# Kernel tuning notes

Measured on AMD Instinct MI355X. Metric: run time of the kernel, lower is better.

The kernel has to match this reference:

```python
import jax, jax.numpy as jnp
import numpy as np

N_NODES = 100000
N_EDGES = 1600000
IN_C = 64
OUT_C = 64
BN_EPS = 1e-5


def setup_inputs() -> dict:
    key = jax.random.key(0)
    k1, k2, k3, k4 = jax.random.split(key, 4)
    x = jax.random.normal(k1, (N_NODES, IN_C), dtype=jnp.float32)
    edge_index = jax.random.randint(k2, (2, N_EDGES), 0, N_NODES, dtype=jnp.int64)
    # GCNConv linear: weight [out, in], bias [out] (PyG default has bias=True)
    W = jax.random.normal(k3, (OUT_C, IN_C), dtype=jnp.float32) / np.sqrt(IN_C)
    b = jax.random.normal(k4, (OUT_C,), dtype=jnp.float32) * 0.01
    # BatchNorm1d affine params
    gamma = jnp.ones((OUT_C,), dtype=jnp.float32)
    beta = jnp.zeros((OUT_C,), dtype=jnp.float32)
    return {"x": x, "edge_index": edge_index, "W": W, "b": b, "gamma": gamma, "beta": beta}


def reference(x, edge_index, W, b, gamma, beta):
    N = x.shape[0]
    # GCNConv: linear transform (no bias yet)
    h = x @ W.T  # [N, out]
    # add self-loops
    loop = jnp.arange(N, dtype=edge_index.dtype)
    src = jnp.concatenate([edge_index[0], loop])  # [E+N]
    dst = jnp.concatenate([edge_index[1], loop])
    # symmetric normalization: deg computed on destination (col)
    ones = jnp.ones(src.shape[0], dtype=h.dtype)
    deg = jax.ops.segment_sum(ones, dst, num_segments=N)  # [N]
    deg_inv_sqrt = jnp.where(deg > 0, jax.lax.rsqrt(deg), 0.0)
    norm = deg_inv_sqrt[src] * deg_inv_sqrt[dst]  # [E+N]
    # gather -> scale -> scatter-add aggregation
    msgs = h[src] * norm[:, None]  # [E+N, out] (dominant memory traffic)
    out = jax.ops.segment_sum(msgs, dst, num_segments=N) + b  # [N, out]
    # BatchNorm1d (training mode: biased batch statistics over nodes)
    mean = out.mean(axis=0)
    var = out.var(axis=0)  # biased, matching torch BN normalization
    y = (out - mean) * jax.lax.rsqrt(var + BN_EPS) * gamma + beta
    return jax.nn.relu(y)
```

## Files before the change

### kernel.cpp

```cpp
#include <hip/hip_runtime.h>
#include <math.h>

#define N_NODES 100000
#define N_EDGES 1600000
#define C 64
#define BN_EPS 1e-5f
#define SLOTS 48

#define WS_HP    0
#define WS_CNT   3200000
#define WS_STAT  3300000
#define WS_SLOT  3300128

#define NPART 8
#define PART_NODES (N_NODES / NPART)
#define NCHUNK 128
#define CHUNK_I4 (N_EDGES / 4 / NCHUNK)

typedef float f4 __attribute__((ext_vector_type(4)));

static __device__ __forceinline__ unsigned short f2bf(float f) {
    unsigned u = __float_as_uint(f);
    unsigned r = 0x7FFFu + ((u >> 16) & 1u);
    return (unsigned short)((u + r) >> 16);
}
static __device__ __forceinline__ float bf2f(unsigned short h) {
    return __uint_as_float(((unsigned)h) << 16);
}

__global__ void r16_scatter(const int* __restrict__ ei, unsigned* __restrict__ cnt,
                            unsigned* __restrict__ slot) {
    const int p  = blockIdx.x & (NPART - 1);
    const int ch = blockIdx.x >> 3;
    const unsigned lo = (unsigned)(p * PART_NODES);
    const unsigned hi = lo + PART_NODES;
    const int4* s4 = reinterpret_cast<const int4*>(ei);
    const int4* d4 = reinterpret_cast<const int4*>(ei + N_EDGES);
    const int beg = ch * CHUNK_I4;
    const int end = beg + CHUNK_I4;
    for (int e = beg + threadIdx.x; e < end; e += 256) {
        int4 d = d4[e];
        int4 s = s4[e];
        unsigned dx = (unsigned)d.x, dy = (unsigned)d.y;
        unsigned dz = (unsigned)d.z, dw = (unsigned)d.w;
        if (dx >= lo && dx < hi) {
            unsigned pos = atomicAdd(&cnt[dx], 1u);
            if (pos < SLOTS) slot[dx * SLOTS + pos] = (unsigned)s.x;
        }
        if (dy >= lo && dy < hi) {
            unsigned pos = atomicAdd(&cnt[dy], 1u);
            if (pos < SLOTS) slot[dy * SLOTS + pos] = (unsigned)s.y;
        }
        if (dz >= lo && dz < hi) {
            unsigned pos = atomicAdd(&cnt[dz], 1u);
            if (pos < SLOTS) slot[dz * SLOTS + pos] = (unsigned)s.z;
        }
        if (dw >= lo && dw < hi) {
            unsigned pos = atomicAdd(&cnt[dw], 1u);
            if (pos < SLOTS) slot[dw * SLOTS + pos] = (unsigned)s.w;
        }
    }
}

__global__ void r16_mm(const float* __restrict__ x, const float* __restrict__ W,
                       const unsigned* __restrict__ cnt, unsigned short* __restrict__ hp) {
    __shared__ float Wt[64 * 65];
    __shared__ float X[16 * 64];
    const int tid = threadIdx.x;
    for (int i = tid; i < 64 * 64; i += 256) {
        float v = W[i];
        Wt[(i & 63) * 65 + (i >> 6)] = v;
    }

    const int c = tid & 63;
    const int w = tid >> 6;
    const int nrow = tid >> 4;
    const int k4 = (tid & 15) << 2;
    const int ngroups = N_NODES / 16;

    for (int g = blockIdx.x; g < ngroups; g += gridDim.x) {
        const int base = g * 16;
        __syncthreads();
        *reinterpret_cast<float4*>(X + nrow * 64 + k4) =
            *reinterpret_cast<const float4*>(x + (base + nrow) * 64 + k4);
        __syncthreads();

        float acc0 = 0.f, acc1 = 0.f, acc2 = 0.f, acc3 = 0.f;
        #pragma unroll
        for (int k = 0; k < 64; k += 4) {
            float w0 = Wt[(k + 0) * 65 + c];
            float w1 = Wt[(k + 1) * 65 + c];
            float w2 = Wt[(k + 2) * 65 + c];
            float w3 = Wt[(k + 3) * 65 + c];
            float4 x0 = *reinterpret_cast<const float4*>(X + (w * 4 + 0) * 64 + k);
            float4 x1 = *reinterpret_cast<const float4*>(X + (w * 4 + 1) * 64 + k);
            float4 x2 = *reinterpret_cast<const float4*>(X + (w * 4 + 2) * 64 + k);
            float4 x3 = *reinterpret_cast<const float4*>(X + (w * 4 + 3) * 64 + k);
            acc0 += x0.x * w0 + x0.y * w1 + x0.z * w2 + x0.w * w3;
            acc1 += x1.x * w0 + x1.y * w1 + x1.z * w2 + x1.w * w3;
            acc2 += x2.x * w0 + x2.y * w1 + x2.z * w2 + x2.w * w3;
            acc3 += x3.x * w0 + x3.y * w1 + x3.z * w2 + x3.w * w3;
        }
        const int n0 = base + w * 4;
        hp[(n0 + 0) * 64 + c] = f2bf(acc0 * rsqrtf((float)(cnt[n0 + 0] + 1u)));
        hp[(n0 + 1) * 64 + c] = f2bf(acc1 * rsqrtf((float)(cnt[n0 + 1] + 1u)));
        hp[(n0 + 2) * 64 + c] = f2bf(acc2 * rsqrtf((float)(cnt[n0 + 2] + 1u)));
        hp[(n0 + 3) * 64 + c] = f2bf(acc3 * rsqrtf((float)(cnt[n0 + 3] + 1u)));
    }
}

__global__ void r16_agg(const unsigned* __restrict__ slot, const unsigned* __restrict__ cnt,
                        const unsigned short* __restrict__ hp, float* __restrict__ out,
                        float* __restrict__ stats) {
    __shared__ float ls[256], lq[256];
    const int tid = threadIdx.x;
    const int c = tid & 63;
    int wid = blockIdx.x * 4 + (tid >> 6);
    const int nw = gridDim.x * 4;
    float s = 0.0f, q = 0.0f;
    for (int n0 = wid * 2; n0 < N_NODES; n0 += nw * 2) {
        const int n1 = n0 + 1;
        unsigned deg0 = cnt[n0], deg1 = cnt[n1];
        int num0 = (deg0 > SLOTS) ? SLOTS : (int)deg0;
        int num1 = (deg1 > SLOTS) ? SLOTS : (int)deg1;
        float dn0 = rsqrtf((float)(deg0 + 1u));
        float dn1 = rsqrtf((float)(deg1 + 1u));
        float acc0 = bf2f(hp[n0 * 64 + c]);
        float acc1 = bf2f(hp[n1 * 64 + c]);
        unsigned p0 = (c < num0) ? slot[n0 * SLOTS + c] : 0u;
        unsigned p1 = (c < num1) ? slot[n1 * SLOTS + c] : 0u;
        const int m = (num0 < num1) ? num0 : num1;
        int j = 0;
        for (; j + 8 <= m; j += 8) {
            unsigned a0 = __shfl(p0, j + 0), a1 = __shfl(p0, j + 1);
            unsigned a2 = __shfl(p0, j + 2), a3 = __shfl(p0, j + 3);
            unsigned a4 = __shfl(p0, j + 4), a5 = __shfl(p0, j + 5);
            unsigned a6 = __shfl(p0, j + 6), a7 = __shfl(p0, j + 7);
            unsigned b0 = __shfl(p1, j + 0), b1 = __shfl(p1, j + 1);
            unsigned b2 = __shfl(p1, j + 2), b3 = __shfl(p1, j + 3);
            unsigned b4 = __shfl(p1, j + 4), b5 = __shfl(p1, j + 5);
            unsigned b6 = __shfl(p1, j + 6), b7 = __shfl(p1, j + 7);
            float fa0 = bf2f(hp[a0 * 64 + c]), fa1 = bf2f(hp[a1 * 64 + c]);
            float fa2 = bf2f(hp[a2 * 64 + c]), fa3 = bf2f(hp[a3 * 64 + c]);
            float fa4 = bf2f(hp[a4 * 64 + c]), fa5 = bf2f(hp[a5 * 64 + c]);
            float fa6 = bf2f(hp[a6 * 64 + c]), fa7 = bf2f(hp[a7 * 64 + c]);
            float fb0 = bf2f(hp[b0 * 64 + c]), fb1 = bf2f(hp[b1 * 64 + c]);
            float fb2 = bf2f(hp[b2 * 64 + c]), fb3 = bf2f(hp[b3 * 64 + c]);
            float fb4 = bf2f(hp[b4 * 64 + c]), fb5 = bf2f(hp[b5 * 64 + c]);
            float fb6 = bf2f(hp[b6 * 64 + c]), fb7 = bf2f(hp[b7 * 64 + c]);
            acc0 += ((fa0 + fa1) + (fa2 + fa3)) + ((fa4 + fa5) + (fa6 + fa7));
            acc1 += ((fb0 + fb1) + (fb2 + fb3)) + ((fb4 + fb5) + (fb6 + fb7));
        }
        int j0 = j, j1 = j;
        for (; j0 + 8 <= num0; j0 += 8) {
            unsigned a0 = __shfl(p0, j0 + 0), a1 = __shfl(p0, j0 + 1);
            unsigned a2 = __shfl(p0, j0 + 2), a3 = __shfl(p0, j0 + 3);
            unsigned a4 = __shfl(p0, j0 + 4), a5 = __shfl(p0, j0 + 5);
            unsigned a6 = __shfl(p0, j0 + 6), a7 = __shfl(p0, j0 + 7);
            float fa0 = bf2f(hp[a0 * 64 + c]), fa1 = bf2f(hp[a1 * 64 + c]);
            float fa2 = bf2f(hp[a2 * 64 + c]), fa3 = bf2f(hp[a3 * 64 + c]);
            float fa4 = bf2f(hp[a4 * 64 + c]), fa5 = bf2f(hp[a5 * 64 + c]);
            float fa6 = bf2f(hp[a6 * 64 + c]), fa7 = bf2f(hp[a7 * 64 + c]);
            acc0 += ((fa0 + fa1) + (fa2 + fa3)) + ((fa4 + fa5) + (fa6 + fa7));
        }
        for (; j1 + 8 <= num1; j1 += 8) {
            unsigned b0 = __shfl(p1, j1 + 0), b1 = __shfl(p1, j1 + 1);
            unsigned b2 = __shfl(p1, j1 + 2), b3 = __shfl(p1, j1 + 3);
            unsigned b4 = __shfl(p1, j1 + 4), b5 = __shfl(p1, j1 + 5);
            unsigned b6 = __shfl(p1, j1 + 6), b7 = __shfl(p1, j1 + 7);
            float fb0 = bf2f(hp[b0 * 64 + c]), fb1 = bf2f(hp[b1 * 64 + c]);
            float fb2 = bf2f(hp[b2 * 64 + c]), fb3 = bf2f(hp[b3 * 64 + c]);
            float fb4 = bf2f(hp[b4 * 64 + c]), fb5 = bf2f(hp[b5 * 64 + c]);
            float fb6 = bf2f(hp[b6 * 64 + c]), fb7 = bf2f(hp[b7 * 64 + c]);
            acc1 += ((fb0 + fb1) + (fb2 + fb3)) + ((fb4 + fb5) + (fb6 + fb7));
        }
        for (; j0 < num0; ++j0) acc0 += bf2f(hp[__shfl(p0, j0) * 64 + c]);
        for (; j1 < num1; ++j1) acc1 += bf2f(hp[__shfl(p1, j1) * 64 + c]);
        float o0 = acc0 * dn0;
        float o1 = acc1 * dn1;
        __builtin_nontemporal_store(o0, &out[n0 * 64 + c]);
        __builtin_nontemporal_store(o1, &out[n1 * 64 + c]);
        s += o0 + o1; q += o0 * o0 + o1 * o1;
    }
    ls[tid] = s; lq[tid] = q;
    __syncthreads();
    if (tid < 64) {
        s = ls[tid] + ls[tid + 64] + ls[tid + 128] + ls[tid + 192];
        q = lq[tid] + lq[tid + 64] + lq[tid + 128] + lq[tid + 192];
        atomicAdd(&stats[tid], s);
        atomicAdd(&stats[64 + tid], q);
    }
}

__global__ void r16_bnrelu(float* __restrict__ out, const float* __restrict__ sum,
                           const float* __restrict__ sq, const float* __restrict__ gamma,
                           const float* __restrict__ beta) {
    int i = blockIdx.x * blockDim.x + threadIdx.x;
    const int st = gridDim.x * blockDim.x;
    const int c0 = (i & 15) << 2;
    float scl[4], sft[4];
    #pragma unroll
    for (int k = 0; k < 4; ++k) {
        float mean = sum[c0 + k] * (1.0f / N_NODES);
        float var  = sq[c0 + k] * (1.0f / N_NODES) - mean * mean;
        float inv  = rsqrtf(var + BN_EPS);
        scl[k] = gamma[c0 + k] * inv;
        sft[k] = beta[c0 + k] - mean * scl[k];
    }
    const int total4 = N_NODES * C / 4;
    f4* o4 = reinterpret_cast<f4*>(out);
    for (; i < total4; i += st) {
        f4 v = __builtin_nontemporal_load(&o4[i]);
        v.x = fmaxf(v.x * scl[0] + sft[0], 0.0f);
        v.y = fmaxf(v.y * scl[1] + sft[1], 0.0f);
        v.z = fmaxf(v.z * scl[2] + sft[2], 0.0f);
        v.w = fmaxf(v.w * scl[3] + sft[3], 0.0f);
        __builtin_nontemporal_store(v, &o4[i]);
    }
}

extern "C" void kernel_launch(void* const* d_in, const int* in_sizes, int n_in,
                              void* d_out, int out_size, void* d_ws, size_t ws_size,
                              hipStream_t stream) {
    const float* x     = (const float*)d_in[0];
    const int*   ei    = (const int*)d_in[1];
    const float* W     = (const float*)d_in[2];
    const float* gamma = (const float*)d_in[4];
    const float* beta  = (const float*)d_in[5];
    float* out = (float*)d_out;
    float*    wsf = (float*)d_ws;
    unsigned* wsu = (unsigned*)d_ws;

    unsigned short* hp = (unsigned short*)(wsf + WS_HP);
    unsigned* cnt   = wsu + WS_CNT;
    float*    stats = wsf + WS_STAT;
    unsigned* slot  = wsu + WS_SLOT;

    hipMemsetAsync(cnt, 0, N_NODES * sizeof(unsigned), stream);
    hipMemsetAsync(stats, 0, 128 * sizeof(float), stream);

    r16_scatter<<<NPART * NCHUNK, 256, 0, stream>>>(ei, cnt, slot);
    r16_mm     <<<832, 256, 0, stream>>>(x, W, cnt, hp);
    r16_agg    <<<4096, 256, 0, stream>>>(slot, cnt, hp, out, stats);
    r16_bnrelu <<<2048, 256, 0, stream>>>(out, stats, stats + 64, gamma, beta);
}
```

Before: 249.8 us.

## Split degree histogram from slot scatter and co-schedule scatter with matmul

```diff
diff --git a/kernel.cpp b/kernel.cpp
--- a/kernel.cpp
+++ b/kernel.cpp
@@ -7,15 +7,18 @@
 #define BN_EPS 1e-5f
 #define SLOTS 48
 
-#define WS_HP    0
-#define WS_CNT   3200000
-#define WS_STAT  3300000
-#define WS_SLOT  3300128
+#define WS_HP     0
+#define WS_CNT    3200000
+#define WS_CURSOR 3300000
+#define WS_STAT   3400000
+#define WS_SLOT   3400128
 
 #define NPART 8
 #define PART_NODES (N_NODES / NPART)
 #define NCHUNK 128
 #define CHUNK_I4 (N_EDGES / 4 / NCHUNK)
+#define NSCAT (NPART * NCHUNK)
+#define NMM   2048
 
 typedef float f4 __attribute__((ext_vector_type(4)));
 
@@ -28,45 +31,60 @@
     return __uint_as_float(((unsigned)h) << 16);
 }
 
-__global__ void r16_scatter(const int* __restrict__ ei, unsigned* __restrict__ cnt,
-                            unsigned* __restrict__ slot) {
-    const int p  = blockIdx.x & (NPART - 1);
-    const int ch = blockIdx.x >> 3;
-    const unsigned lo = (unsigned)(p * PART_NODES);
-    const unsigned hi = lo + PART_NODES;
-    const int4* s4 = reinterpret_cast<const int4*>(ei);
+__global__ void r17_hist(const int* __restrict__ ei, unsigned* __restrict__ cnt) {
+    int i = blockIdx.x * blockDim.x + threadIdx.x;
+    const int st = gridDim.x * blockDim.x;
     const int4* d4 = reinterpret_cast<const int4*>(ei + N_EDGES);
-    const int beg = ch * CHUNK_I4;
-    const int end = beg + CHUNK_I4;
-    for (int e = beg + threadIdx.x; e < end; e += 256) {
-        int4 d = d4[e];
-        int4 s = s4[e];
-        unsigned dx = (unsigned)d.x, dy = (unsigned)d.y;
-        unsigned dz = (unsigned)d.z, dw = (unsigned)d.w;
-        if (dx >= lo && dx < hi) {
-            unsigned pos = atomicAdd(&cnt[dx], 1u);
-            if (pos < SLOTS) slot[dx * SLOTS + pos] = (unsigned)s.x;
-        }
-        if (dy >= lo && dy < hi) {
-            unsigned pos = atomicAdd(&cnt[dy], 1u);
-            if (pos < SLOTS) slot[dy * SLOTS + pos] = (unsigned)s.y;
-        }
-        if (dz >= lo && dz < hi) {
-            unsigned pos = atomicAdd(&cnt[dz], 1u);
-            if (pos < SLOTS) slot[dz * SLOTS + pos] = (unsigned)s.z;
-        }
-        if (dw >= lo && dw < hi) {
-            unsigned pos = atomicAdd(&cnt[dw], 1u);
-            if (pos < SLOTS) slot[dw * SLOTS + pos] = (unsigned)s.w;
-        }
-    }
-}
-
-__global__ void r16_mm(const float* __restrict__ x, const float* __restrict__ W,
-                       const unsigned* __restrict__ cnt, unsigned short* __restrict__ hp) {
+    for (int e = i; e < N_EDGES / 4; e += st) {
+        int4 v = d4[e];
+        atomicAdd(&cnt[v.x], 1u); atomicAdd(&cnt[v.y], 1u);
+        atomicAdd(&cnt[v.z], 1u); atomicAdd(&cnt[v.w], 1u);
+    }
+}
+
+__global__ void r17_fused(const int* __restrict__ ei, const unsigned* __restrict__ cnt,
+                          unsigned* __restrict__ cursor, unsigned* __restrict__ slot,
+                          const float* __restrict__ x, const float* __restrict__ W,
+                          unsigned short* __restrict__ hp) {
     __shared__ float Wt[64 * 65];
     __shared__ float X[16 * 64];
     const int tid = threadIdx.x;
+
+    if (blockIdx.x < NSCAT) {
+        const int p  = blockIdx.x & (NPART - 1);
+        const int ch = blockIdx.x >> 3;
+        const unsigned lo = (unsigned)(p * PART_NODES);
+        const unsigned hi = lo + PART_NODES;
+        const int4* s4 = reinterpret_cast<const int4*>(ei);
+        const int4* d4 = reinterpret_cast<const int4*>(ei + N_EDGES);
+        const int beg = ch * CHUNK_I4;
+        const int end = beg + CHUNK_I4;
+        for (int e = beg + tid; e < end; e += 256) {
+            int4 d = d4[e];
+            int4 s = s4[e];
+            unsigned dx = (unsigned)d.x, dy = (unsigned)d.y;
+            unsigned dz = (unsigned)d.z, dw = (unsigned)d.w;
+            if (dx >= lo && dx < hi) {
+                unsigned pos = atomicAdd(&cursor[dx], 1u);
+                if (pos < SLOTS) slot[dx * SLOTS + pos] = (unsigned)s.x;
+            }
+            if (dy >= lo && dy < hi) {
+                unsigned pos = atomicAdd(&cursor[dy], 1u);
+                if (pos < SLOTS) slot[dy * SLOTS + pos] = (unsigned)s.y;
+            }
+            if (dz >= lo && dz < hi) {
+                unsigned pos = atomicAdd(&cursor[dz], 1u);
+                if (pos < SLOTS) slot[dz * SLOTS + pos] = (unsigned)s.z;
+            }
+            if (dw >= lo && dw < hi) {
+                unsigned pos = atomicAdd(&cursor[dw], 1u);
+                if (pos < SLOTS) slot[dw * SLOTS + pos] = (unsigned)s.w;
+            }
+        }
+        return;
+    }
+
+    const int bid = blockIdx.x - NSCAT;
     for (int i = tid; i < 64 * 64; i += 256) {
         float v = W[i];
         Wt[(i & 63) * 65 + (i >> 6)] = v;
@@ -78,7 +96,7 @@
     const int k4 = (tid & 15) << 2;
     const int ngroups = N_NODES / 16;
 
-    for (int g = blockIdx.x; g < ngroups; g += gridDim.x) {
+    for (int g = bid; g < ngroups; g += NMM) {
         const int base = g * 16;
         __syncthreads();
         *reinterpret_cast<float4*>(X + nrow * 64 + k4) =
@@ -109,7 +127,7 @@
     }
 }
 
-__global__ void r16_agg(const unsigned* __restrict__ slot, const unsigned* __restrict__ cnt,
+__global__ void r17_agg(const unsigned* __restrict__ slot, const unsigned* __restrict__ cnt,
                         const unsigned short* __restrict__ hp, float* __restrict__ out,
                         float* __restrict__ stats) {
     __shared__ float ls[256], lq[256];
@@ -192,7 +210,7 @@
     }
 }
 
-__global__ void r16_bnrelu(float* __restrict__ out, const float* __restrict__ sum,
+__global__ void r17_bnrelu(float* __restrict__ out, const float* __restrict__ sum,
                            const float* __restrict__ sq, const float* __restrict__ gamma,
                            const float* __restrict__ beta) {
     int i = blockIdx.x * blockDim.x + threadIdx.x;
@@ -232,15 +250,16 @@
     unsigned* wsu = (unsigned*)d_ws;
 
     unsigned short* hp = (unsigned short*)(wsf + WS_HP);
-    unsigned* cnt   = wsu + WS_CNT;
-    float*    stats = wsf + WS_STAT;
-    unsigned* slot  = wsu + WS_SLOT;
-
-    hipMemsetAsync(cnt, 0, N_NODES * sizeof(unsigned), stream);
+    unsigned* cnt    = wsu + WS_CNT;
+    unsigned* cursor = wsu + WS_CURSOR;
+    float*    stats  = wsf + WS_STAT;
+    unsigned* slot   = wsu + WS_SLOT;
+
+    hipMemsetAsync(cnt, 0, 2 * N_NODES * sizeof(unsigned), stream);
     hipMemsetAsync(stats, 0, 128 * sizeof(float), stream);
 
-    r16_scatter<<<NPART * NCHUNK, 256, 0, stream>>>(ei, cnt, slot);
-    r16_mm     <<<832, 256, 0, stream>>>(x, W, cnt, hp);
-    r16_agg    <<<4096, 256, 0, stream>>>(slot, cnt, hp, out, stats);
-    r16_bnrelu <<<2048, 256, 0, stream>>>(out, stats, stats + 64, gamma, beta);
-}
+    r17_hist  <<<1024, 256, 0, stream>>>(ei, cnt);
+    r17_fused <<<NSCAT + NMM, 256, 0, stream>>>(ei, cnt, cursor, slot, x, W, hp);
+    r17_agg   <<<4096, 256, 0, stream>>>(slot, cnt, hp, out, stats);
+    r17_bnrelu<<<2048, 256, 0, stream>>>(out, stats, stats + 64, gamma, beta);
+}
```

Result: slower. 302.6 us (+21.2%).
